# Kernel optimization log

Hardware: AMD Instinct MI355X
Metric: run time of the kernel (lower is better)

## Reference

```python
import math
import jax, jax.numpy as jnp
import numpy as np

N, E = 20000, 640000
S_DIM, Z_DIM, H, QK, VD = 64, 64, 4, 8, 8
EPS = 1e-8


def quat_rotate(v, q):
    # v: [..., 3], q: [..., 4] (w, x, y, z), broadcastable. Unit-quaternion rotation:
    # v' = v + 2*(w*(u x v) + u x (u x v))
    w = q[..., 0:1]
    u = q[..., 1:4]
    uv = jnp.cross(u, v)
    return v + 2.0 * (w * uv + jnp.cross(u, uv))


def setup_inputs() -> dict:
    key = jax.random.key(0)
    ks = jax.random.split(key, 16)
    s = jax.random.normal(ks[0], (N, S_DIM), dtype=jnp.float32)
    z = jax.random.normal(ks[1], (E, Z_DIM), dtype=jnp.float32)
    edge_index = jax.random.randint(ks[2], (2, E), 0, N)
    quaternion = jax.random.normal(ks[3], (N, 4), dtype=jnp.float32)
    quaternion = quaternion / jnp.linalg.norm(quaternion, axis=-1, keepdims=True)
    translation = jax.random.normal(ks[4], (N, 3), dtype=jnp.float32)
    sc_s = 1.0 / math.sqrt(S_DIM)
    sc_z = 1.0 / math.sqrt(Z_DIM)
    # weights stored [in, out] so y = x @ W (equivalent to torch x @ W.T)
    Wq_s = jax.random.normal(ks[5], (S_DIM, H * S_DIM), dtype=jnp.float32) * sc_s
    Wk_s = jax.random.normal(ks[6], (S_DIM, H * S_DIM), dtype=jnp.float32) * sc_s
    Wv_s = jax.random.normal(ks[7], (S_DIM, H * S_DIM), dtype=jnp.float32) * sc_s
    Wq_v = jax.random.normal(ks[8], (S_DIM, H * QK * 3), dtype=jnp.float32) * sc_s
    Wk_v = jax.random.normal(ks[9], (S_DIM, H * QK * 3), dtype=jnp.float32) * sc_s
    Wv_v = jax.random.normal(ks[10], (S_DIM, H * VD * 3), dtype=jnp.float32) * sc_s
    Wb = jax.random.normal(ks[11], (Z_DIM, H), dtype=jnp.float32) * sc_z
    bb = jnp.zeros((H,), dtype=jnp.float32)
    Wdz = jax.random.normal(ks[12], (Z_DIM, Z_DIM // 4), dtype=jnp.float32) * sc_z
    bdz = jnp.zeros((Z_DIM // 4,), dtype=jnp.float32)
    head_weights = jnp.full((H,), 0.541324854612918, dtype=jnp.float32)  # softplus^{-1}(1)
    concat_dim = Z_DIM // 4 + S_DIM + VD * 4
    Wout = jax.random.normal(ks[13], (H * concat_dim, S_DIM), dtype=jnp.float32) / math.sqrt(H * concat_dim)
    bout = jnp.zeros((S_DIM,), dtype=jnp.float32)
    return {
        's': s, 'z': z, 'edge_index': edge_index, 'quaternion': quaternion,
        'translation': translation, 'Wq_s': Wq_s, 'Wk_s': Wk_s, 'Wv_s': Wv_s,
        'Wq_v': Wq_v, 'Wk_v': Wk_v, 'Wv_v': Wv_v, 'Wb': Wb, 'bb': bb,
        'Wdz': Wdz, 'bdz': bdz, 'head_weights': head_weights,
        'Wout': Wout, 'bout': bout,
    }


def reference(s, z, edge_index, quaternion, translation,
              Wq_s, Wk_s, Wv_s, Wq_v, Wk_v, Wv_v,
              Wb, bb, Wdz, bdz, head_weights, Wout, bout):
    idx_i, idx_j = edge_index[0], edge_index[1]
    n = s.shape[0]
    h = head_weights.shape[0]
    qk = Wq_v.shape[1] // (3 * h)
    vd = Wv_v.shape[1] // (3 * h)

    q_scalar = (s @ Wq_s).reshape(n, h, -1)
    k_scalar = (s @ Wk_s).reshape(n, h, -1)
    v_scalar = (s @ Wv_s).reshape(n, h, -1)

    def to_points(x):
        # torch.split into 3 chunks then stack(dim=-1): [n, 3*c] -> [n, c, 3]
        c = x.shape[-1] // 3
        return jnp.swapaxes(x.reshape(n, 3, c), 1, 2)

    quat_b = quaternion[:, None, :]
    trans_b = translation[:, None, :]
    q_vec = (quat_rotate(to_points(s @ Wq_v), quat_b) + trans_b).reshape(n, h, qk, 3)
    k_vec = (quat_rotate(to_points(s @ Wk_v), quat_b) + trans_b).reshape(n, h, qk, 3)
    v_vec = (quat_rotate(to_points(s @ Wv_v), quat_b) + trans_b).reshape(n, h, vd, 3)

    b_bias = z @ Wb + bb  # [E, H]

    attn = jnp.sum(k_scalar[idx_i] * q_scalar[idx_j], axis=-1)  # [E, H]
    attn = attn * math.sqrt(1.0 / 3 * qk) + math.sqrt(1.0 / 3) * b_bias

    disp = q_vec[idx_i] - k_vec[idx_j]            # [E, H, qk, 3]
    vec_att = jnp.sum(disp * disp, axis=-1)       # [E, H, qk]
    hw = jax.nn.softplus(head_weights)[None, :, None]
    vec_att = jnp.sum(vec_att * hw, axis=-1) * math.sqrt(1.0 / (3 * (qk * 9.0 / 2))) * (-0.5)
    attn = attn + vec_att

    # segment softmax over destination node idx_i
    seg_max = jax.ops.segment_max(attn, idx_i, num_segments=n)
    ea = jnp.exp(attn - seg_max[idx_i])
    denom = jax.ops.segment_sum(ea, idx_i, num_segments=n)
    attn = ea / denom[idx_i]                      # [E, H]

    out_scalar = jax.ops.segment_sum(attn[:, :, None] * v_scalar[idx_i], idx_i, num_segments=n)
    out_scalar = out_scalar.reshape(n, -1)

    out_vec = jax.ops.segment_sum(attn[:, :, None, None] * v_vec[idx_i], idx_i, num_segments=n)
    out_vec = out_vec - translation[:, None, None, :]
    q_conj = jnp.concatenate([quaternion[:, :1], -quaternion[:, 1:]], axis=-1)
    out_vec = quat_rotate(out_vec, q_conj[:, None, None, :])   # [n, h, vd, 3]
    out_vec_norm = jnp.sqrt(jnp.sum(out_vec * out_vec, axis=-1) + EPS).reshape(n, -1)
    out_vec_flat = out_vec.reshape(n, -1, 3)

    pair_z = z @ Wdz + bdz                         # [E, z/4]
    out_pair = jax.ops.segment_sum(attn[:, :, None] * pair_z[:, None, :], idx_i, num_segments=n)
    out_pair = out_pair.reshape(n, -1)

    feats = jnp.concatenate([out_scalar,
                             out_vec_flat[..., 0], out_vec_flat[..., 1], out_vec_flat[..., 2],
                             out_vec_norm, out_pair], axis=-1)
    return feats @ Wout + bout
```

## Files before the change

kernel.cpp:

```cpp
#include <hip/hip_runtime.h>
#include <stdint.h>


#define C_SQRT83  1.6329931618554518f
#define C_SQRT13  0.5773502691896258f
#define C_VEC    -0.04811252243246881f

__device__ __forceinline__ unsigned short f2bf(float f){
  unsigned u = __float_as_uint(f);
  u += 0x7fffu + ((u >> 16) & 1u);
  return (unsigned short)(u >> 16);
}
__device__ __forceinline__ unsigned pack2(float a, float b){
  return (unsigned)f2bf(a) | ((unsigned)f2bf(b) << 16);
}
__device__ __forceinline__ float bflo(unsigned u){ return __uint_as_float(u << 16); }
__device__ __forceinline__ float bfhi(unsigned u){ return __uint_as_float(u & 0xffff0000u); }

__device__ __forceinline__ void quat_rot(float w, float ux, float uy, float uz,
                                         float vx, float vy, float vz,
                                         float& ox, float& oy, float& oz){
  float cx = uy*vz - uz*vy;
  float cy = uz*vx - ux*vz;
  float cz = ux*vy - uy*vx;
  float dx = uy*cz - uz*cy;
  float dy = uz*cx - ux*cz;
  float dz = ux*cy - uy*cx;
  ox = vx + 2.f*(w*cx + dx);
  oy = vy + 2.f*(w*cy + dy);
  oz = vz + 2.f*(w*cz + dz);
}


__global__ __launch_bounds__(256) void k_count(const int* __restrict__ ei,
                                               unsigned* __restrict__ counts,
                                               unsigned* __restrict__ rank, int ne){
  int e = blockIdx.x*256 + threadIdx.x;
  if (e >= ne) return;
  rank[e] = atomicAdd(&counts[ei[e]], 1u);
}

__global__ __launch_bounds__(256) void k_scan(const unsigned* __restrict__ counts,
                                              unsigned* __restrict__ row_off, int n){
  __shared__ unsigned part[256];
  int t = threadIdx.x;
  int chunk = (n + 255) >> 8;
  int s0 = t*chunk, s1 = min(s0 + chunk, n);
  unsigned sum = 0;
  for (int k = s0; k < s1; ++k) sum += counts[k];
  part[t] = sum; __syncthreads();
  for (int off = 1; off < 256; off <<= 1){
    unsigned v = (t >= off) ? part[t-off] : 0u;
    __syncthreads();
    part[t] += v;
    __syncthreads();
  }
  unsigned run = (t == 0) ? 0u : part[t-1];
  for (int k = s0; k < s1; ++k){
    row_off[k] = run; run += counts[k];
  }
  if (t == 255) row_off[n] = part[255];
}


__global__ __launch_bounds__(256) void k_zfill(
    const int* __restrict__ ei, const unsigned* __restrict__ rank,
    const unsigned* __restrict__ roff, const float* __restrict__ z,
    const float* __restrict__ Wb,  const float* __restrict__ bb,
    const float* __restrict__ Wdz, const float* __restrict__ bdz,
    unsigned* __restrict__ si, unsigned* __restrict__ sj,
    float* __restrict__ logits, unsigned* __restrict__ pz, int ne)
{
  const int e = blockIdx.x*256 + threadIdx.x;
  if (e >= ne) return;
  const int i = ei[e];
  const unsigned pos = roff[i] + rank[e];
  si[pos] = (unsigned)i;
  sj[pos] = (unsigned)ei[ne + e];

  float b4[4];  b4[0]=b4[1]=b4[2]=b4[3]=0.f;
  float pacc[16];
  #pragma unroll
  for (int c=0;c<16;c++) pacc[c]=0.f;
  const float* zr = z + (size_t)e*64;
  #pragma unroll
  for (int k4 = 0; k4 < 16; ++k4){
    const float4 zv = *(const float4*)(zr + 4*k4);
    #pragma unroll
    for (int kk = 0; kk < 4; ++kk){
      const int k = 4*k4 + kk;
      const float zk = (kk==0)?zv.x:((kk==1)?zv.y:((kk==2)?zv.z:zv.w));
      const float4 wb = *(const float4*)(Wb + k*4);
      b4[0]+=zk*wb.x; b4[1]+=zk*wb.y; b4[2]+=zk*wb.z; b4[3]+=zk*wb.w;
      const float* wd = Wdz + k*16;
      const float4 w0=*(const float4*)(wd), w1=*(const float4*)(wd+4),
                   w2=*(const float4*)(wd+8), w3=*(const float4*)(wd+12);
      pacc[ 0]+=zk*w0.x; pacc[ 1]+=zk*w0.y; pacc[ 2]+=zk*w0.z; pacc[ 3]+=zk*w0.w;
      pacc[ 4]+=zk*w1.x; pacc[ 5]+=zk*w1.y; pacc[ 6]+=zk*w1.z; pacc[ 7]+=zk*w1.w;
      pacc[ 8]+=zk*w2.x; pacc[ 9]+=zk*w2.y; pacc[10]+=zk*w2.z; pacc[11]+=zk*w2.w;
      pacc[12]+=zk*w3.x; pacc[13]+=zk*w3.y; pacc[14]+=zk*w3.z; pacc[15]+=zk*w3.w;
    }
  }
  #pragma unroll
  for (int c=0;c<16;c++) pacc[c] += bdz[c];
  { uint4 u0, u1;
    u0.x=pack2(pacc[0],pacc[1]);   u0.y=pack2(pacc[2],pacc[3]);
    u0.z=pack2(pacc[4],pacc[5]);   u0.w=pack2(pacc[6],pacc[7]);
    u1.x=pack2(pacc[8],pacc[9]);   u1.y=pack2(pacc[10],pacc[11]);
    u1.z=pack2(pacc[12],pacc[13]); u1.w=pack2(pacc[14],pacc[15]);
    uint4* d = (uint4*)(pz + (size_t)pos*8);
    d[0]=u0; d[1]=u1; }

  float4 bo;
  bo.x = C_SQRT13*(b4[0] + bb[0]);
  bo.y = C_SQRT13*(b4[1] + bb[1]);
  bo.z = C_SQRT13*(b4[2] + bb[2]);
  bo.w = C_SQRT13*(b4[3] + bb[3]);
  *(float4*)(logits + (size_t)pos*4) = bo;
}


#define BN 32

__device__ __forceinline__ void pass256(const float* __restrict__ W,
                                        const float stT[64][40], int cg, int sl,
                                        float acc[8][4]){
  #pragma unroll
  for (int i=0;i<8;i++){ acc[i][0]=0.f; acc[i][1]=0.f; acc[i][2]=0.f; acc[i][3]=0.f; }
  #pragma unroll 4
  for (int k = 0; k < 64; ++k){
    const float4 w  = *(const float4*)(W + (size_t)k*256 + cg*4);
    const float4 n0 = *(const float4*)&stT[k][sl*8];
    const float4 n1 = *(const float4*)&stT[k][sl*8+4];
    acc[0][0]+=n0.x*w.x; acc[0][1]+=n0.x*w.y; acc[0][2]+=n0.x*w.z; acc[0][3]+=n0.x*w.w;
    acc[1][0]+=n0.y*w.x; acc[1][1]+=n0.y*w.y; acc[1][2]+=n0.y*w.z; acc[1][3]+=n0.y*w.w;
    acc[2][0]+=n0.z*w.x; acc[2][1]+=n0.z*w.y; acc[2][2]+=n0.z*w.z; acc[2][3]+=n0.z*w.w;
    acc[3][0]+=n0.w*w.x; acc[3][1]+=n0.w*w.y; acc[3][2]+=n0.w*w.z; acc[3][3]+=n0.w*w.w;
    acc[4][0]+=n1.x*w.x; acc[4][1]+=n1.x*w.y; acc[4][2]+=n1.x*w.z; acc[4][3]+=n1.x*w.w;
    acc[5][0]+=n1.y*w.x; acc[5][1]+=n1.y*w.y; acc[5][2]+=n1.y*w.z; acc[5][3]+=n1.y*w.w;
    acc[6][0]+=n1.z*w.x; acc[6][1]+=n1.z*w.y; acc[6][2]+=n1.z*w.z; acc[6][3]+=n1.z*w.w;
    acc[7][0]+=n1.w*w.x; acc[7][1]+=n1.w*w.y; acc[7][2]+=n1.w*w.z; acc[7][3]+=n1.w*w.w;
  }
}

__device__ __forceinline__ void pass96(const float* __restrict__ W,
                                       const float stT[64][40], int cgp, int slp,
                                       float acc[4][4]){
  #pragma unroll
  for (int i=0;i<4;i++){ acc[i][0]=0.f; acc[i][1]=0.f; acc[i][2]=0.f; acc[i][3]=0.f; }
  if (cgp >= 24) return;
  #pragma unroll 4
  for (int k = 0; k < 64; ++k){
    const float4 w = *(const float4*)(W + (size_t)k*96 + cgp*4);
    const float4 nv = *(const float4*)&stT[k][slp*4];
    acc[0][0]+=nv.x*w.x; acc[0][1]+=nv.x*w.y; acc[0][2]+=nv.x*w.z; acc[0][3]+=nv.x*w.w;
    acc[1][0]+=nv.y*w.x; acc[1][1]+=nv.y*w.y; acc[1][2]+=nv.y*w.z; acc[1][3]+=nv.y*w.w;
    acc[2][0]+=nv.z*w.x; acc[2][1]+=nv.z*w.y; acc[2][2]+=nv.z*w.z; acc[2][3]+=nv.z*w.w;
    acc[3][0]+=nv.w*w.x; acc[3][1]+=nv.w*w.y; acc[3][2]+=nv.w*w.z; acc[3][3]+=nv.w*w.w;
  }
}

__global__ __launch_bounds__(256) void k_proj(
    const float* __restrict__ s, const float* __restrict__ quat, const float* __restrict__ trans,
    const float* __restrict__ Wqs, const float* __restrict__ Wks, const float* __restrict__ Wvs,
    const float* __restrict__ Wqv, const float* __restrict__ Wkv, const float* __restrict__ Wvv,
    unsigned* __restrict__ qs, unsigned* __restrict__ ks, float* __restrict__ vs,
    unsigned* __restrict__ qv, unsigned* __restrict__ kv, float* __restrict__ vv, int n)
{
  __shared__ float stT[64][40];
  __shared__ float pt[BN][97];
  const int tid = threadIdx.x;
  const int node0 = blockIdx.x * BN;

  #pragma unroll
  for (int r = 0; r < 2; ++r){
    const int idx = tid + r*256;
    const int nd = idx >> 4, c4 = idx & 15;
    const int g = node0 + nd;
    float4 v = make_float4(0.f,0.f,0.f,0.f);
    if (g < n) v = *(const float4*)(s + (size_t)g*64 + c4*4);
    stT[c4*4+0][nd]=v.x; stT[c4*4+1][nd]=v.y; stT[c4*4+2][nd]=v.z; stT[c4*4+3][nd]=v.w;
  }
  __syncthreads();

  const int cg = tid & 63, sl = tid >> 6;
  const int cgp = tid & 31, slp = tid >> 5;
  float acc[8][4];

  pass256(Wqs, stT, cg, sl, acc);
  #pragma unroll
  for (int i=0;i<8;i++){
    const int g = node0 + sl*8 + i;
    if (g < n){
      uint2 u; u.x = pack2(acc[i][0],acc[i][1]); u.y = pack2(acc[i][2],acc[i][3]);
      *(uint2*)(qs + (size_t)g*128 + cg*2) = u;
    }
  }
  pass256(Wks, stT, cg, sl, acc);
  #pragma unroll
  for (int i=0;i<8;i++){
    const int g = node0 + sl*8 + i;
    if (g < n){
      uint2 u; u.x = pack2(acc[i][0],acc[i][1]); u.y = pack2(acc[i][2],acc[i][3]);
      *(uint2*)(ks + (size_t)g*128 + cg*2) = u;
    }
  }
  pass256(Wvs, stT, cg, sl, acc);
  #pragma unroll
  for (int i=0;i<8;i++){
    const int g = node0 + sl*8 + i;
    if (g < n){
      float4 f; f.x=acc[i][0]; f.y=acc[i][1]; f.z=acc[i][2]; f.w=acc[i][3];
      *(float4*)(vs + (size_t)g*256 + cg*4) = f;
    }
  }

  float pac[4][4];

  pass96(Wqv, stT, cgp, slp, pac);
  __syncthreads();
  if (cgp < 24){
    #pragma unroll
    for (int i=0;i<4;i++){
      #pragma unroll
      for (int c=0;c<4;c++) pt[slp*4+i][cgp*4+c] = pac[i][c];
    }
  }
  __syncthreads();
  #pragma unroll
  for (int r = 0; r < 2; ++r){
    const int t2 = tid + r*256;
    const int nd = t2 >> 4, pp = t2 & 15;
    const int g = node0 + nd;
    if (g < n){
      const float4 q4 = *(const float4*)(quat + (size_t)g*4);
      const float tx = trans[(size_t)g*3], ty = trans[(size_t)g*3+1], tz = trans[(size_t)g*3+2];
      float x0,y0,z0,x1,y1,z1;
      quat_rot(q4.x,q4.y,q4.z,q4.w, pt[nd][2*pp],   pt[nd][32+2*pp],   pt[nd][64+2*pp],   x0,y0,z0);
      quat_rot(q4.x,q4.y,q4.z,q4.w, pt[nd][2*pp+1], pt[nd][32+2*pp+1], pt[nd][64+2*pp+1], x1,y1,z1);
      x0+=tx; y0+=ty; z0+=tz; x1+=tx; y1+=ty; z1+=tz;
      unsigned* d = qv + (size_t)g*48 + pp*3;
      d[0] = pack2(x0,y0); d[1] = pack2(z0,x1); d[2] = pack2(y1,z1);
    }
  }

  pass96(Wkv, stT, cgp, slp, pac);
  __syncthreads();
  if (cgp < 24){
    #pragma unroll
    for (int i=0;i<4;i++){
      #pragma unroll
      for (int c=0;c<4;c++) pt[slp*4+i][cgp*4+c] = pac[i][c];
    }
  }
  __syncthreads();
  #pragma unroll
  for (int r = 0; r < 2; ++r){
    const int t2 = tid + r*256;
    const int nd = t2 >> 4, pp = t2 & 15;
    const int g = node0 + nd;
    if (g < n){
      const float4 q4 = *(const float4*)(quat + (size_t)g*4);
      const float tx = trans[(size_t)g*3], ty = trans[(size_t)g*3+1], tz = trans[(size_t)g*3+2];
      float x0,y0,z0,x1,y1,z1;
      quat_rot(q4.x,q4.y,q4.z,q4.w, pt[nd][2*pp],   pt[nd][32+2*pp],   pt[nd][64+2*pp],   x0,y0,z0);
      quat_rot(q4.x,q4.y,q4.z,q4.w, pt[nd][2*pp+1], pt[nd][32+2*pp+1], pt[nd][64+2*pp+1], x1,y1,z1);
      x0+=tx; y0+=ty; z0+=tz; x1+=tx; y1+=ty; z1+=tz;
      unsigned* d = kv + (size_t)g*48 + pp*3;
      d[0] = pack2(x0,y0); d[1] = pack2(z0,x1); d[2] = pack2(y1,z1);
    }
  }

  pass96(Wvv, stT, cgp, slp, pac);
  __syncthreads();
  if (cgp < 24){
    #pragma unroll
    for (int i=0;i<4;i++){
      #pragma unroll
      for (int c=0;c<4;c++) pt[slp*4+i][cgp*4+c] = pac[i][c];
    }
  }
  __syncthreads();
  #pragma unroll
  for (int r = 0; r < 12; ++r){
    const int idx = tid + r*256;
    const int nd = idx / 96, col = idx - nd*96;
    const int g = node0 + nd;
    if (g < n) vv[(size_t)g*96 + col] = pt[nd][col];
  }
}


__global__ __launch_bounds__(256) void k_edge(
    const unsigned* __restrict__ si, const unsigned* __restrict__ sj,
    const float* __restrict__ hwts,
    const unsigned* __restrict__ qs, const unsigned* __restrict__ ks,
    const unsigned* __restrict__ qv, const unsigned* __restrict__ kv,
    float* __restrict__ logits, int ne)
{
  const int p = blockIdx.x*256 + threadIdx.x;
  if (p >= ne) return;
  const unsigned i = si[p], j = sj[p];

  const float4 bias = *(const float4*)(logits + (size_t)p*4);

  const uint4* kr = (const uint4*)(ks + (size_t)i*128);
  const uint4* qr = (const uint4*)(qs + (size_t)j*128);
  float sdot[4];
  #pragma unroll
  for (int h = 0; h < 4; ++h){
    float acc = 0.f;
    #pragma unroll
    for (int c = 0; c < 8; ++c){
      const uint4 a = kr[h*8+c];
      const uint4 b = qr[h*8+c];
      acc += bflo(a.x)*bflo(b.x) + bfhi(a.x)*bfhi(b.x);
      acc += bflo(a.y)*bflo(b.y) + bfhi(a.y)*bfhi(b.y);
      acc += bflo(a.z)*bflo(b.z) + bfhi(a.z)*bfhi(b.z);
      acc += bflo(a.w)*bflo(b.w) + bfhi(a.w)*bfhi(b.w);
    }
    sdot[h] = acc;
  }

  const uint4* qvr = (const uint4*)(qv + (size_t)i*48);
  const uint4* kvr = (const uint4*)(kv + (size_t)j*48);
  float vsum[4];
  #pragma unroll
  for (int h = 0; h < 4; ++h){
    float acc = 0.f;
    #pragma unroll
    for (int c = 0; c < 3; ++c){
      const uint4 a = qvr[h*3+c];
      const uint4 b = kvr[h*3+c];
      float d;
      d = bflo(a.x)-bflo(b.x); acc += d*d;  d = bfhi(a.x)-bfhi(b.x); acc += d*d;
      d = bflo(a.y)-bflo(b.y); acc += d*d;  d = bfhi(a.y)-bfhi(b.y); acc += d*d;
      d = bflo(a.z)-bflo(b.z); acc += d*d;  d = bfhi(a.z)-bfhi(b.z); acc += d*d;
      d = bflo(a.w)-bflo(b.w); acc += d*d;  d = bfhi(a.w)-bfhi(b.w); acc += d*d;
    }
    vsum[h] = acc;
  }

  float4 lg;
  {
    float l[4];
    const float4 b4 = bias;
    const float bb4[4] = {b4.x, b4.y, b4.z, b4.w};
    #pragma unroll
    for (int h = 0; h < 4; ++h){
      const float hw = log1pf(__expf(hwts[h]));
      l[h] = C_SQRT83*sdot[h] + bb4[h] + C_VEC*hw*vsum[h];
    }
    lg.x=l[0]; lg.y=l[1]; lg.z=l[2]; lg.w=l[3];
  }
  *(float4*)(logits + (size_t)p*4) = lg;
}


__global__ __launch_bounds__(256) void k_soft(
    const float* __restrict__ logits, const unsigned* __restrict__ pz,
    const unsigned* __restrict__ row_off, float* __restrict__ out_pair, int n)
{
  const int node = blockIdx.x*4 + (threadIdx.x >> 6);
  if (node >= n) return;
  const int lane = threadIdx.x & 63;
  const int beg = (int)row_off[node], end = (int)row_off[node+1];

  float m[4] = {-3.0e38f,-3.0e38f,-3.0e38f,-3.0e38f};
  for (int p = beg + lane; p < end; p += 64){
    const float4 l = *(const float4*)(logits + (size_t)p*4);
    m[0]=fmaxf(m[0],l.x); m[1]=fmaxf(m[1],l.y); m[2]=fmaxf(m[2],l.z); m[3]=fmaxf(m[3],l.w);
  }
  #pragma unroll
  for (int msk = 1; msk < 64; msk <<= 1){
    #pragma unroll
    for (int h=0;h<4;h++) m[h] = fmaxf(m[h], __shfl_xor(m[h], msk));
  }
  float S[4] = {0.f,0.f,0.f,0.f};
  for (int p = beg + lane; p < end; p += 64){
    const float4 l = *(const float4*)(logits + (size_t)p*4);
    S[0]+=__expf(l.x-m[0]); S[1]+=__expf(l.y-m[1]);
    S[2]+=__expf(l.z-m[2]); S[3]+=__expf(l.w-m[3]);
  }
  #pragma unroll
  for (int msk = 1; msk < 64; msk <<= 1){
    #pragma unroll
    for (int h=0;h<4;h++) S[h] += __shfl_xor(S[h], msk);
  }
  float inv[4];
  #pragma unroll
  for (int h=0;h<4;h++) inv[h] = (S[h] > 0.f) ? (1.f/S[h]) : 0.f;

  const int e4 = lane >> 4, c = lane & 15;
  float acc[4] = {0.f,0.f,0.f,0.f};
  for (int base = beg; base < end; base += 4){
    const int p = base + e4;
    if (p < end){
      const float4 l = *(const float4*)(logits + (size_t)p*4);
      const unsigned u = pz[(size_t)p*8 + (c>>1)];
      const float pzv = (c & 1) ? bfhi(u) : bflo(u);
      acc[0] += __expf(l.x-m[0]) * pzv;
      acc[1] += __expf(l.y-m[1]) * pzv;
      acc[2] += __expf(l.z-m[2]) * pzv;
      acc[3] += __expf(l.w-m[3]) * pzv;
    }
  }
  #pragma unroll
  for (int msk = 16; msk < 64; msk <<= 1){
    #pragma unroll
    for (int h=0;h<4;h++) acc[h] += __shfl_xor(acc[h], msk);
  }
  const int hOut = lane >> 4;
  out_pair[(size_t)node*64 + lane] = acc[hOut] * inv[hOut];
}


__global__ __launch_bounds__(256) void k_out(
    const float* __restrict__ vs, const float* __restrict__ vv,
    const float* __restrict__ out_pair, const unsigned* __restrict__ row_off,
    const float* __restrict__ quat, const float* __restrict__ trans,
    const float* __restrict__ Wout, const float* __restrict__ bout,
    float* __restrict__ out, int n)
{
  __shared__ float feats[32][448];
  __shared__ int degs[32];
  const int tid = threadIdx.x;
  const int node0 = blockIdx.x*32;

  if (tid < 32){
    const int g = node0 + tid;
    degs[tid] = (g < n) ? (int)(row_off[g+1] - row_off[g]) : 1;
  }
  __syncthreads();

  for (int x = tid; x < 32*256; x += 256){
    const int nd = x >> 8, c = x & 255;
    const int g = node0 + nd;
    feats[nd][c] = (g < n && degs[nd] > 0) ? vs[(size_t)g*256 + c] : 0.f;
  }
  for (int x = tid; x < 32*64; x += 256){
    const int nd = x >> 6, c = x & 63;
    const int g = node0 + nd;
    feats[nd][384 + c] = (g < n) ? out_pair[(size_t)g*64 + c] : 0.f;
  }
  for (int x = tid; x < 32*32; x += 256){
    const int nd = x >> 5, pt = x & 31;
    const int g = node0 + nd;
    float X=0.f, Y=0.f, Z=0.f;
    if (g < n){
      if (degs[nd] > 0){
        X = vv[(size_t)g*96 + pt];
        Y = vv[(size_t)g*96 + 32 + pt];
        Z = vv[(size_t)g*96 + 64 + pt];
      } else {
        const float4 q4 = *(const float4*)(quat + (size_t)g*4);
        const float tx = trans[(size_t)g*3], ty = trans[(size_t)g*3+1], tz = trans[(size_t)g*3+2];
        quat_rot(q4.x, -q4.y, -q4.z, -q4.w, -tx, -ty, -tz, X, Y, Z);
      }
    }
    feats[nd][256 + pt] = X;
    feats[nd][288 + pt] = Y;
    feats[nd][320 + pt] = Z;
    feats[nd][352 + pt] = sqrtf(X*X + Y*Y + Z*Z + 1e-8f);
  }
  __syncthreads();

  const int lane = tid & 63;
  const int wave = tid >> 6;
  float acc[8];
  #pragma unroll
  for (int q8=0;q8<8;q8++) acc[q8]=0.f;

  for (int k0 = 0; k0 < 448; k0 += 4){
    const float w0 = Wout[(size_t)(k0+0)*64 + lane];
    const float w1 = Wout[(size_t)(k0+1)*64 + lane];
    const float w2 = Wout[(size_t)(k0+2)*64 + lane];
    const float w3 = Wout[(size_t)(k0+3)*64 + lane];
    #pragma unroll
    for (int q8 = 0; q8 < 8; ++q8){
      const float4 f = *(const float4*)&feats[wave*8 + q8][k0];
      acc[q8] += f.x*w0 + f.y*w1 + f.z*w2 + f.w*w3;
    }
  }
  const float bo = bout[lane];
  #pragma unroll
  for (int q8 = 0; q8 < 8; ++q8){
    const int g = node0 + wave*8 + q8;
    if (g < n) out[(size_t)g*64 + lane] = acc[q8] + bo;
  }
}


extern "C" void kernel_launch(void* const* d_in, const int* in_sizes, int n_in,
                              void* d_out, int out_size, void* d_ws, size_t ws_size,
                              hipStream_t stream) {
  const float* s     = (const float*)d_in[0];
  const float* z     = (const float*)d_in[1];
  const int*   ei    = (const int*)  d_in[2];
  const float* quat  = (const float*)d_in[3];
  const float* trans = (const float*)d_in[4];
  const float* Wqs   = (const float*)d_in[5];
  const float* Wks   = (const float*)d_in[6];
  const float* Wvs   = (const float*)d_in[7];
  const float* Wqv   = (const float*)d_in[8];
  const float* Wkv   = (const float*)d_in[9];
  const float* Wvv   = (const float*)d_in[10];
  const float* Wb    = (const float*)d_in[11];
  const float* bb    = (const float*)d_in[12];
  const float* Wdz   = (const float*)d_in[13];
  const float* bdz   = (const float*)d_in[14];
  const float* hwts  = (const float*)d_in[15];
  const float* Wout  = (const float*)d_in[16];
  const float* bout  = (const float*)d_in[17];
  float* out = (float*)d_out;

  const int n  = in_sizes[0] / 64;
  const int ne = in_sizes[1] / 64;

  size_t off = 0;
  char* base = (char*)d_ws;
  auto take = [&](size_t bytes)->char* {
    char* p = base + off;
    off += (bytes + 255) & ~(size_t)255;
    return p;
  };
  unsigned* qs     = (unsigned*)take((size_t)n*512);
  unsigned* ks     = (unsigned*)take((size_t)n*512);
  unsigned* qvt    = (unsigned*)take((size_t)n*192);
  unsigned* kvt    = (unsigned*)take((size_t)n*192);
  float*    vs     = (float*)   take((size_t)n*1024);
  float*    vv     = (float*)   take((size_t)n*384);
  float*    logits = (float*)   take((size_t)ne*16);
  unsigned* pz     = (unsigned*)take((size_t)ne*32);
  unsigned* counts = (unsigned*)take((size_t)n*4);
  unsigned* roff   = (unsigned*)take((size_t)(n+1)*4);
  unsigned* rank   = (unsigned*)take((size_t)ne*4);
  unsigned* si     = (unsigned*)take((size_t)ne*4);
  unsigned* sj     = (unsigned*)take((size_t)ne*4);
  float*    opair  = (float*)   take((size_t)n*256);
  (void)ws_size; (void)n_in; (void)out_size;

  const int gbE = (ne + 255) / 256;

  hipMemsetAsync(counts, 0, (size_t)n*4, stream);
  k_count<<<gbE, 256, 0, stream>>>(ei, counts, rank, ne);
  k_scan <<<1,   256, 0, stream>>>(counts, roff, n);
  k_zfill<<<gbE, 256, 0, stream>>>(ei, rank, roff, z, Wb, bb, Wdz, bdz,
                                   si, sj, logits, pz, ne);
  k_proj <<<(n + BN - 1)/BN, 256, 0, stream>>>(s, quat, trans, Wqs, Wks, Wvs, Wqv, Wkv, Wvv,
                                               qs, ks, vs, qvt, kvt, vv, n);
  k_edge <<<gbE, 256, 0, stream>>>(si, sj, hwts, qs, ks, qvt, kvt, logits, ne);
  k_soft <<<(n + 3)/4, 256, 0, stream>>>(logits, pz, roff, opair, n);
  k_out  <<<(n + 31)/32, 256, 0, stream>>>(vs, vv, opair, roff, quat, trans,
                                           Wout, bout, out, n);
}
```

Baseline: 702.1 us.

## Fuse z projection and edge logits into one kernel with packed per-edge records

Merges the z-projection/scatter kernel and the edge-logit kernel into a single kernel, so the si/sj index arrays and the separate logits read-back are no longer needed. The z tile is staged through shared memory with a transpose and double buffering to get coalesced loads. The q·k and vector-distance gathers are cooperatively split across 4 lanes per edge, with shuffle reductions. Logits and bf16 pair features are written into one 64-byte record per edge, which the softmax kernel reads. This costs extra shuffles and shared memory, and gathers now run in edge order rather than sorted order, which may reduce node-row locality.

```diff
diff --git a/kernel.cpp b/kernel.cpp
--- a/kernel.cpp
+++ b/kernel.cpp
@@ -63,63 +63,6 @@
 }
 
 
-__global__ __launch_bounds__(256) void k_zfill(
-    const int* __restrict__ ei, const unsigned* __restrict__ rank,
-    const unsigned* __restrict__ roff, const float* __restrict__ z,
-    const float* __restrict__ Wb,  const float* __restrict__ bb,
-    const float* __restrict__ Wdz, const float* __restrict__ bdz,
-    unsigned* __restrict__ si, unsigned* __restrict__ sj,
-    float* __restrict__ logits, unsigned* __restrict__ pz, int ne)
-{
-  const int e = blockIdx.x*256 + threadIdx.x;
-  if (e >= ne) return;
-  const int i = ei[e];
-  const unsigned pos = roff[i] + rank[e];
-  si[pos] = (unsigned)i;
-  sj[pos] = (unsigned)ei[ne + e];
-
-  float b4[4];  b4[0]=b4[1]=b4[2]=b4[3]=0.f;
-  float pacc[16];
-  #pragma unroll
-  for (int c=0;c<16;c++) pacc[c]=0.f;
-  const float* zr = z + (size_t)e*64;
-  #pragma unroll
-  for (int k4 = 0; k4 < 16; ++k4){
-    const float4 zv = *(const float4*)(zr + 4*k4);
-    #pragma unroll
-    for (int kk = 0; kk < 4; ++kk){
-      const int k = 4*k4 + kk;
-      const float zk = (kk==0)?zv.x:((kk==1)?zv.y:((kk==2)?zv.z:zv.w));
-      const float4 wb = *(const float4*)(Wb + k*4);
-      b4[0]+=zk*wb.x; b4[1]+=zk*wb.y; b4[2]+=zk*wb.z; b4[3]+=zk*wb.w;
-      const float* wd = Wdz + k*16;
-      const float4 w0=*(const float4*)(wd), w1=*(const float4*)(wd+4),
-                   w2=*(const float4*)(wd+8), w3=*(const float4*)(wd+12);
-      pacc[ 0]+=zk*w0.x; pacc[ 1]+=zk*w0.y; pacc[ 2]+=zk*w0.z; pacc[ 3]+=zk*w0.w;
-      pacc[ 4]+=zk*w1.x; pacc[ 5]+=zk*w1.y; pacc[ 6]+=zk*w1.z; pacc[ 7]+=zk*w1.w;
-      pacc[ 8]+=zk*w2.x; pacc[ 9]+=zk*w2.y; pacc[10]+=zk*w2.z; pacc[11]+=zk*w2.w;
-      pacc[12]+=zk*w3.x; pacc[13]+=zk*w3.y; pacc[14]+=zk*w3.z; pacc[15]+=zk*w3.w;
-    }
-  }
-  #pragma unroll
-  for (int c=0;c<16;c++) pacc[c] += bdz[c];
-  { uint4 u0, u1;
-    u0.x=pack2(pacc[0],pacc[1]);   u0.y=pack2(pacc[2],pacc[3]);
-    u0.z=pack2(pacc[4],pacc[5]);   u0.w=pack2(pacc[6],pacc[7]);
-    u1.x=pack2(pacc[8],pacc[9]);   u1.y=pack2(pacc[10],pacc[11]);
-    u1.z=pack2(pacc[12],pacc[13]); u1.w=pack2(pacc[14],pacc[15]);
-    uint4* d = (uint4*)(pz + (size_t)pos*8);
-    d[0]=u0; d[1]=u1; }
-
-  float4 bo;
-  bo.x = C_SQRT13*(b4[0] + bb[0]);
-  bo.y = C_SQRT13*(b4[1] + bb[1]);
-  bo.z = C_SQRT13*(b4[2] + bb[2]);
-  bo.w = C_SQRT13*(b4[3] + bb[3]);
-  *(float4*)(logits + (size_t)pos*4) = bo;
-}
-
-
 #define BN 32
 
 __device__ __forceinline__ void pass256(const float* __restrict__ W,
@@ -291,84 +234,262 @@
 }
 
 
-__global__ __launch_bounds__(256) void k_edge(
-    const unsigned* __restrict__ si, const unsigned* __restrict__ sj,
+__global__ __launch_bounds__(256) void k_zc(
+    const int* __restrict__ ei, const unsigned* __restrict__ rank,
+    const unsigned* __restrict__ roff, const float* __restrict__ z,
+    const float* __restrict__ Wb,  const float* __restrict__ bb,
+    const float* __restrict__ Wdz, const float* __restrict__ bdz,
     const float* __restrict__ hwts,
     const unsigned* __restrict__ qs, const unsigned* __restrict__ ks,
     const unsigned* __restrict__ qv, const unsigned* __restrict__ kv,
-    float* __restrict__ logits, int ne)
+    unsigned* __restrict__ rec, int ne)
 {
-  const int p = blockIdx.x*256 + threadIdx.x;
-  if (p >= ne) return;
-  const unsigned i = si[p], j = sj[p];
-
-  const float4 bias = *(const float4*)(logits + (size_t)p*4);
-
-  const uint4* kr = (const uint4*)(ks + (size_t)i*128);
-  const uint4* qr = (const uint4*)(qs + (size_t)j*128);
-  float sdot[4];
-  #pragma unroll
-  for (int h = 0; h < 4; ++h){
-    float acc = 0.f;
-    #pragma unroll
-    for (int c = 0; c < 8; ++c){
-      const uint4 a = kr[h*8+c];
-      const uint4 b = qr[h*8+c];
-      acc += bflo(a.x)*bflo(b.x) + bfhi(a.x)*bfhi(b.x);
-      acc += bflo(a.y)*bflo(b.y) + bfhi(a.y)*bfhi(b.y);
-      acc += bflo(a.z)*bflo(b.z) + bfhi(a.z)*bfhi(b.z);
-      acc += bflo(a.w)*bflo(b.w) + bfhi(a.w)*bfhi(b.w);
-    }
-    sdot[h] = acc;
-  }
-
-  const uint4* qvr = (const uint4*)(qv + (size_t)i*48);
-  const uint4* kvr = (const uint4*)(kv + (size_t)j*48);
-  float vsum[4];
-  #pragma unroll
-  for (int h = 0; h < 4; ++h){
-    float acc = 0.f;
-    #pragma unroll
-    for (int c = 0; c < 3; ++c){
-      const uint4 a = qvr[h*3+c];
-      const uint4 b = kvr[h*3+c];
-      float d;
-      d = bflo(a.x)-bflo(b.x); acc += d*d;  d = bfhi(a.x)-bfhi(b.x); acc += d*d;
-      d = bflo(a.y)-bflo(b.y); acc += d*d;  d = bfhi(a.y)-bfhi(b.y); acc += d*d;
-      d = bflo(a.z)-bflo(b.z); acc += d*d;  d = bfhi(a.z)-bfhi(b.z); acc += d*d;
-      d = bflo(a.w)-bflo(b.w); acc += d*d;  d = bfhi(a.w)-bfhi(b.w); acc += d*d;
-    }
-    vsum[h] = acc;
-  }
-
-  float4 lg;
-  {
-    float l[4];
-    const float4 b4 = bias;
-    const float bb4[4] = {b4.x, b4.y, b4.z, b4.w};
+  __shared__ float zT[2][16][258];
+  const int tid = threadIdx.x;
+  const int E0  = blockIdx.x * 256;
+  const int e   = E0 + tid;
+  const bool full = (E0 + 256 <= ne);
+
+  int i = 0, j = 0; unsigned pos = 0;
+  if (e < ne){
+    i = ei[e]; j = ei[ne + e];
+    pos = roff[i] + rank[e];
+  }
+
+  const float hw0 = C_VEC * log1pf(__expf(hwts[0]));
+  const float hw1 = C_VEC * log1pf(__expf(hwts[1]));
+  const float hw2 = C_VEC * log1pf(__expf(hwts[2]));
+  const float hw3 = C_VEC * log1pf(__expf(hwts[3]));
+
+  float b4[4] = {0.f,0.f,0.f,0.f};
+  float pacc[16];
+  #pragma unroll
+  for (int c=0;c<16;c++) pacc[c]=0.f;
+
+  if (full){
+    #pragma unroll
+    for (int q = 0; q < 4; ++q){
+      const int idx = tid + q*256;
+      const int row = idx >> 2, f4 = idx & 3;
+      const float4 v = *(const float4*)(z + (size_t)(E0+row)*64 + f4*4);
+      zT[0][f4*4+0][row]=v.x; zT[0][f4*4+1][row]=v.y;
+      zT[0][f4*4+2][row]=v.z; zT[0][f4*4+3][row]=v.w;
+    }
+    __syncthreads();
+    #pragma unroll
+    for (int c = 0; c < 4; ++c){
+      if (c < 3){
+        const int nb = (c+1)&1;
+        #pragma unroll
+        for (int q = 0; q < 4; ++q){
+          const int idx = tid + q*256;
+          const int row = idx >> 2, f4 = idx & 3;
+          const float4 v = *(const float4*)(z + (size_t)(E0+row)*64 + (c+1)*16 + f4*4);
+          zT[nb][f4*4+0][row]=v.x; zT[nb][f4*4+1][row]=v.y;
+          zT[nb][f4*4+2][row]=v.z; zT[nb][f4*4+3][row]=v.w;
+        }
+      }
+      const int kb = c*16, buf = c&1;
+      #pragma unroll
+      for (int kk = 0; kk < 16; ++kk){
+        const float zk = zT[buf][kk][tid];
+        const int k = kb + kk;
+        const float4 wb = *(const float4*)(Wb + k*4);
+        b4[0]+=zk*wb.x; b4[1]+=zk*wb.y; b4[2]+=zk*wb.z; b4[3]+=zk*wb.w;
+        const float* wd = Wdz + k*16;
+        const float4 w0=*(const float4*)(wd),   w1=*(const float4*)(wd+4),
+                     w2=*(const float4*)(wd+8), w3=*(const float4*)(wd+12);
+        pacc[ 0]+=zk*w0.x; pacc[ 1]+=zk*w0.y; pacc[ 2]+=zk*w0.z; pacc[ 3]+=zk*w0.w;
+        pacc[ 4]+=zk*w1.x; pacc[ 5]+=zk*w1.y; pacc[ 6]+=zk*w1.z; pacc[ 7]+=zk*w1.w;
+        pacc[ 8]+=zk*w2.x; pacc[ 9]+=zk*w2.y; pacc[10]+=zk*w2.z; pacc[11]+=zk*w2.w;
+        pacc[12]+=zk*w3.x; pacc[13]+=zk*w3.y; pacc[14]+=zk*w3.z; pacc[15]+=zk*w3.w;
+      }
+      __syncthreads();
+    }
+  } else if (e < ne){
+    const float* zr = z + (size_t)e*64;
+    for (int k4 = 0; k4 < 16; ++k4){
+      const float4 zv = *(const float4*)(zr + 4*k4);
+      #pragma unroll
+      for (int kk = 0; kk < 4; ++kk){
+        const int k = 4*k4 + kk;
+        const float zk = (kk==0)?zv.x:((kk==1)?zv.y:((kk==2)?zv.z:zv.w));
+        const float4 wb = *(const float4*)(Wb + k*4);
+        b4[0]+=zk*wb.x; b4[1]+=zk*wb.y; b4[2]+=zk*wb.z; b4[3]+=zk*wb.w;
+        const float* wd = Wdz + k*16;
+        const float4 w0=*(const float4*)(wd),   w1=*(const float4*)(wd+4),
+                     w2=*(const float4*)(wd+8), w3=*(const float4*)(wd+12);
+        pacc[ 0]+=zk*w0.x; pacc[ 1]+=zk*w0.y; pacc[ 2]+=zk*w0.z; pacc[ 3]+=zk*w0.w;
+        pacc[ 4]+=zk*w1.x; pacc[ 5]+=zk*w1.y; pacc[ 6]+=zk*w1.z; pacc[ 7]+=zk*w1.w;
+        pacc[ 8]+=zk*w2.x; pacc[ 9]+=zk*w2.y; pacc[10]+=zk*w2.z; pacc[11]+=zk*w2.w;
+        pacc[12]+=zk*w3.x; pacc[13]+=zk*w3.y; pacc[14]+=zk*w3.z; pacc[15]+=zk*w3.w;
+      }
+    }
+  }
+
+  uint4 u0, u1;
+  float bl0=0.f, bl1=0.f, bl2=0.f, bl3=0.f;
+  if (e < ne){
+    #pragma unroll
+    for (int c=0;c<16;c++) pacc[c] += bdz[c];
+    u0.x=pack2(pacc[0],pacc[1]);   u0.y=pack2(pacc[2],pacc[3]);
+    u0.z=pack2(pacc[4],pacc[5]);   u0.w=pack2(pacc[6],pacc[7]);
+    u1.x=pack2(pacc[8],pacc[9]);   u1.y=pack2(pacc[10],pacc[11]);
+    u1.z=pack2(pacc[12],pacc[13]); u1.w=pack2(pacc[14],pacc[15]);
+    bl0 = C_SQRT13*(b4[0] + bb[0]);
+    bl1 = C_SQRT13*(b4[1] + bb[1]);
+    bl2 = C_SQRT13*(b4[2] + bb[2]);
+    bl3 = C_SQRT13*(b4[3] + bb[3]);
+  } else {
+    u0 = make_uint4(0,0,0,0); u1 = make_uint4(0,0,0,0);
+  }
+
+  if (full){
+    const int l = tid & 63;
+    const int c = l & 3, g = l >> 2;
+    #pragma unroll
+    for (int sb = 0; sb < 4; ++sb){
+      const int el = sb*16 + g;
+      const int ie = __shfl(i, el, 64);
+      const int je = __shfl(j, el, 64);
+
+      const uint4* kr = (const uint4*)ks + (size_t)ie*32;
+      const uint4* qr = (const uint4*)qs + (size_t)je*32;
+      float s0=0.f, s1=0.f, s2=0.f, s3=0.f;
+      #pragma unroll
+      for (int it = 0; it < 8; ++it){
+        const uint4 a = kr[it*4 + c];
+        const uint4 b = qr[it*4 + c];
+        float d;
+        d  = bflo(a.x)*bflo(b.x) + bfhi(a.x)*bfhi(b.x);
+        d += bflo(a.y)*bflo(b.y) + bfhi(a.y)*bfhi(b.y);
+        d += bflo(a.z)*bflo(b.z) + bfhi(a.z)*bfhi(b.z);
+        d += bflo(a.w)*bflo(b.w) + bfhi(a.w)*bfhi(b.w);
+        if      (it < 2) s0 += d;
+        else if (it < 4) s1 += d;
+        else if (it < 6) s2 += d;
+        else             s3 += d;
+      }
+
+      const uint4* qvr = (const uint4*)qv + (size_t)ie*12;
+      const uint4* kvr = (const uint4*)kv + (size_t)je*12;
+      float v0=0.f, v1=0.f, v2=0.f, v3=0.f;
+      {
+        const uint4 a = qvr[c], b = kvr[c];
+        float d, t;
+        t = bflo(a.x)-bflo(b.x); d  = t*t;  t = bfhi(a.x)-bfhi(b.x); d += t*t;
+        t = bflo(a.y)-bflo(b.y); d += t*t;  t = bfhi(a.y)-bfhi(b.y); d += t*t;
+        t = bflo(a.z)-bflo(b.z); d += t*t;  t = bfhi(a.z)-bfhi(b.z); d += t*t;
+        t = bflo(a.w)-bflo(b.w); d += t*t;  t = bfhi(a.w)-bfhi(b.w); d += t*t;
+        if (c < 3) v0 += d; else v1 += d;
+      }
+      {
+        const uint4 a = qvr[4+c], b = kvr[4+c];
+        float d, t;
+        t = bflo(a.x)-bflo(b.x); d  = t*t;  t = bfhi(a.x)-bfhi(b.x); d += t*t;
+        t = bflo(a.y)-bflo(b.y); d += t*t;  t = bfhi(a.y)-bfhi(b.y); d += t*t;
+        t = bflo(a.z)-bflo(b.z); d += t*t;  t = bfhi(a.z)-bfhi(b.z); d += t*t;
+        t = bflo(a.w)-bflo(b.w); d += t*t;  t = bfhi(a.w)-bfhi(b.w); d += t*t;
+        if (c < 2) v1 += d; else v2 += d;
+      }
+      {
+        const uint4 a = qvr[8+c], b = kvr[8+c];
+        float d, t;
+        t = bflo(a.x)-bflo(b.x); d  = t*t;  t = bfhi(a.x)-bfhi(b.x); d += t*t;
+        t = bflo(a.y)-bflo(b.y); d += t*t;  t = bfhi(a.y)-bfhi(b.y); d += t*t;
+        t = bflo(a.z)-bflo(b.z); d += t*t;  t = bfhi(a.z)-bfhi(b.z); d += t*t;
+        t = bflo(a.w)-bflo(b.w); d += t*t;  t = bfhi(a.w)-bfhi(b.w); d += t*t;
+        if (c < 1) v2 += d; else v3 += d;
+      }
+
+      float p0 = C_SQRT83*s0 + hw0*v0;
+      float p1 = C_SQRT83*s1 + hw1*v1;
+      float p2 = C_SQRT83*s2 + hw2*v2;
+      float p3 = C_SQRT83*s3 + hw3*v3;
+      #pragma unroll
+      for (int msk = 1; msk < 4; msk <<= 1){
+        p0 += __shfl_xor(p0, msk, 64);
+        p1 += __shfl_xor(p1, msk, 64);
+        p2 += __shfl_xor(p2, msk, 64);
+        p3 += __shfl_xor(p3, msk, 64);
+      }
+      const float pc = (c==0)?p0:((c==1)?p1:((c==2)?p2:p3));
+
+      const int srcbase = (l & 15) << 2;
+      const float q0 = __shfl(pc, srcbase+0, 64);
+      const float q1 = __shfl(pc, srcbase+1, 64);
+      const float q2 = __shfl(pc, srcbase+2, 64);
+      const float q3 = __shfl(pc, srcbase+3, 64);
+      if ((l >> 4) == sb){
+        uint4* d = (uint4*)rec + (size_t)pos*4;
+        float4 lg; lg.x = q0 + bl0; lg.y = q1 + bl1; lg.z = q2 + bl2; lg.w = q3 + bl3;
+        d[0] = *(uint4*)&lg;
+        d[1] = u0;
+        d[2] = u1;
+      }
+    }
+  } else if (e < ne){
+    const uint4* kr = (const uint4*)ks + (size_t)i*32;
+    const uint4* qr = (const uint4*)qs + (size_t)j*32;
+    float sdot[4];
     #pragma unroll
     for (int h = 0; h < 4; ++h){
-      const float hw = log1pf(__expf(hwts[h]));
-      l[h] = C_SQRT83*sdot[h] + bb4[h] + C_VEC*hw*vsum[h];
-    }
-    lg.x=l[0]; lg.y=l[1]; lg.z=l[2]; lg.w=l[3];
-  }
-  *(float4*)(logits + (size_t)p*4) = lg;
+      float acc = 0.f;
+      #pragma unroll
+      for (int cc = 0; cc < 8; ++cc){
+        const uint4 a = kr[h*8+cc];
+        const uint4 b = qr[h*8+cc];
+        acc += bflo(a.x)*bflo(b.x) + bfhi(a.x)*bfhi(b.x);
+        acc += bflo(a.y)*bflo(b.y) + bfhi(a.y)*bfhi(b.y);
+        acc += bflo(a.z)*bflo(b.z) + bfhi(a.z)*bfhi(b.z);
+        acc += bflo(a.w)*bflo(b.w) + bfhi(a.w)*bfhi(b.w);
+      }
+      sdot[h] = acc;
+    }
+    const uint4* qvr = (const uint4*)qv + (size_t)i*12;
+    const uint4* kvr = (const uint4*)kv + (size_t)j*12;
+    float vsum[4];
+    #pragma unroll
+    for (int h = 0; h < 4; ++h){
+      float acc = 0.f;
+      #pragma unroll
+      for (int cc = 0; cc < 3; ++cc){
+        const uint4 a = qvr[h*3+cc];
+        const uint4 b = kvr[h*3+cc];
+        float d;
+        d = bflo(a.x)-bflo(b.x); acc += d*d;  d = bfhi(a.x)-bfhi(b.x); acc += d*d;
+        d = bflo(a.y)-bflo(b.y); acc += d*d;  d = bfhi(a.y)-bfhi(b.y); acc += d*d;
+        d = bflo(a.z)-bflo(b.z); acc += d*d;  d = bfhi(a.z)-bfhi(b.z); acc += d*d;
+        d = bflo(a.w)-bflo(b.w); acc += d*d;  d = bfhi(a.w)-bfhi(b.w); acc += d*d;
+      }
+      vsum[h] = acc;
+    }
+    float4 lg;
+    lg.x = C_SQRT83*sdot[0] + bl0 + hw0*vsum[0];
+    lg.y = C_SQRT83*sdot[1] + bl1 + hw1*vsum[1];
+    lg.z = C_SQRT83*sdot[2] + bl2 + hw2*vsum[2];
+    lg.w = C_SQRT83*sdot[3] + bl3 + hw3*vsum[3];
+    uint4* d = (uint4*)rec + (size_t)pos*4;
+    d[0] = *(uint4*)&lg;
+    d[1] = u0;
+    d[2] = u1;
+  }
 }
 
 
 __global__ __launch_bounds__(256) void k_soft(
-    const float* __restrict__ logits, const unsigned* __restrict__ pz,
+    const unsigned* __restrict__ rec,
     const unsigned* __restrict__ row_off, float* __restrict__ out_pair, int n)
 {
   const int node = blockIdx.x*4 + (threadIdx.x >> 6);
   if (node >= n) return;
   const int lane = threadIdx.x & 63;
   const int beg = (int)row_off[node], end = (int)row_off[node+1];
+  const float* recf = (const float*)rec;
 
   float m[4] = {-3.0e38f,-3.0e38f,-3.0e38f,-3.0e38f};
   for (int p = beg + lane; p < end; p += 64){
-    const float4 l = *(const float4*)(logits + (size_t)p*4);
+    const float4 l = *(const float4*)(recf + (size_t)p*16);
     m[0]=fmaxf(m[0],l.x); m[1]=fmaxf(m[1],l.y); m[2]=fmaxf(m[2],l.z); m[3]=fmaxf(m[3],l.w);
   }
   #pragma unroll
@@ -378,7 +499,7 @@
   }
   float S[4] = {0.f,0.f,0.f,0.f};
   for (int p = beg + lane; p < end; p += 64){
-    const float4 l = *(const float4*)(logits + (size_t)p*4);
+    const float4 l = *(const float4*)(recf + (size_t)p*16);
     S[0]+=__expf(l.x-m[0]); S[1]+=__expf(l.y-m[1]);
     S[2]+=__expf(l.z-m[2]); S[3]+=__expf(l.w-m[3]);
   }
@@ -396,8 +517,8 @@
   for (int base = beg; base < end; base += 4){
     const int p = base + e4;
     if (p < end){
-      const float4 l = *(const float4*)(logits + (size_t)p*4);
-      const unsigned u = pz[(size_t)p*8 + (c>>1)];
+      const float4 l = *(const float4*)(recf + (size_t)p*16);
+      const unsigned u = rec[(size_t)p*16 + 4 + (c>>1)];
       const float pzv = (c & 1) ? bfhi(u) : bflo(u);
       acc[0] += __expf(l.x-m[0]) * pzv;
       acc[1] += __expf(l.y-m[1]) * pzv;
@@ -530,13 +651,10 @@
   unsigned* kvt    = (unsigned*)take((size_t)n*192);
   float*    vs     = (float*)   take((size_t)n*1024);
   float*    vv     = (float*)   take((size_t)n*384);
-  float*    logits = (float*)   take((size_t)ne*16);
-  unsigned* pz     = (unsigned*)take((size_t)ne*32);
+  unsigned* rec    = (unsigned*)take((size_t)ne*64);
   unsigned* counts = (unsigned*)take((size_t)n*4);
   unsigned* roff   = (unsigned*)take((size_t)(n+1)*4);
   unsigned* rank   = (unsigned*)take((size_t)ne*4);
-  unsigned* si     = (unsigned*)take((size_t)ne*4);
-  unsigned* sj     = (unsigned*)take((size_t)ne*4);
   float*    opair  = (float*)   take((size_t)n*256);
   (void)ws_size; (void)n_in; (void)out_size;
 
@@ -545,12 +663,11 @@
   hipMemsetAsync(counts, 0, (size_t)n*4, stream);
   k_count<<<gbE, 256, 0, stream>>>(ei, counts, rank, ne);
   k_scan <<<1,   256, 0, stream>>>(counts, roff, n);
-  k_zfill<<<gbE, 256, 0, stream>>>(ei, rank, roff, z, Wb, bb, Wdz, bdz,
-                                   si, sj, logits, pz, ne);
   k_proj <<<(n + BN - 1)/BN, 256, 0, stream>>>(s, quat, trans, Wqs, Wks, Wvs, Wqv, Wkv, Wvv,
                                                qs, ks, vs, qvt, kvt, vv, n);
-  k_edge <<<gbE, 256, 0, stream>>>(si, sj, hwts, qs, ks, qvt, kvt, logits, ne);
-  k_soft <<<(n + 3)/4, 256, 0, stream>>>(logits, pz, roff, opair, n);
+  k_zc   <<<gbE, 256, 0, stream>>>(ei, rank, roff, z, Wb, bb, Wdz, bdz, hwts,
+                                   qs, ks, qvt, kvt, rec, ne);
+  k_soft <<<(n + 3)/4, 256, 0, stream>>>(rec, roff, opair, n);
   k_out  <<<(n + 31)/32, 256, 0, stream>>>(vs, vv, opair, roff, quat, trans,
                                            Wout, bout, out, n);
 }
```

After: 617.0 us. -12.1%, faster.
